# Optimization experiments

Hardware: AMD Instinct MI355X
Metric: run time of the kernel (lower is better)

Reference implementation:

```python
import jax, jax.numpy as jnp
import numpy as np
import math

EPS = 1e-5

def _ln(x, w, b):
    m = jnp.mean(x, axis=-1, keepdims=True)
    v = jnp.mean((x - m) ** 2, axis=-1, keepdims=True)
    return (x - m) * jax.lax.rsqrt(v + EPS) * w + b

def setup_inputs() -> dict:
    key = jax.random.key(0)
    L, E, V, T, B = 8, 1024, 32000, 1024, 4
    ks = jax.random.split(key, 9)
    f = lambda k, s: jax.random.normal(k, s, dtype=jnp.float32) * 0.02
    return dict(
        idx=jax.random.randint(ks[0], (B, T), 0, V),
        wte=f(ks[1], (V, E)),
        wpe=f(ks[2], (T, E)),
        ln1_w=jnp.ones((L, E), jnp.float32), ln1_b=jnp.zeros((L, E), jnp.float32),
        attn_w=f(ks[3], (L, 3 * E, E)), attn_b=jnp.zeros((L, 3 * E), jnp.float32),
        proj_w=f(ks[4], (L, E, E)), proj_b=jnp.zeros((L, E), jnp.float32),
        ln2_w=jnp.ones((L, E), jnp.float32), ln2_b=jnp.zeros((L, E), jnp.float32),
        fc_w=f(ks[5], (L, 4 * E, E)), fc_b=jnp.zeros((L, 4 * E), jnp.float32),
        fc2_w=f(ks[6], (L, E, 4 * E)), fc2_b=jnp.zeros((L, E), jnp.float32),
        lnf_w=jnp.ones((E,), jnp.float32), lnf_b=jnp.zeros((E,), jnp.float32),
        lm_head_w=f(ks[7], (V, E)),
        n_head=16,
    )

def reference(idx, wte, wpe, ln1_w, ln1_b, attn_w, attn_b, proj_w, proj_b,
              ln2_w, ln2_b, fc_w, fc_b, fc2_w, fc2_b, lnf_w, lnf_b,
              lm_head_w, n_head):
    B, T = idx.shape
    E = wte.shape[1]
    H = int(n_head)
    hd = E // H
    scale = 1.0 / math.sqrt(hd)
    x = wte[idx] + wpe[:T]  # [B,T,E]
    causal = jnp.tril(jnp.ones((T, T), dtype=bool))
    neg_inf = jnp.float32(-jnp.inf)

    def body(x, p):
        l1w, l1b, Wa, ba, Wp, bp, l2w, l2b, Wf, bf, W2, b2 = p
        h = _ln(x, l1w, l1b)
        qkv = h @ Wa.T + ba  # [B,T,3E]
        q, k, v = jnp.split(qkv, 3, axis=-1)
        q = q.reshape(B, T, H, hd)
        k = k.reshape(B, T, H, hd)
        v = v.reshape(B, T, H, hd)
        att = jnp.einsum('bqhd,bkhd->bhqk', q, k) * scale
        att = jnp.where(causal, att, neg_inf)
        att = jax.nn.softmax(att, axis=-1)  # dropout is identity in eval
        y = jnp.einsum('bhqk,bkhd->bqhd', att, v).reshape(B, T, E)
        x = x + (y @ Wp.T + bp)
        h2 = _ln(x, l2w, l2b)
        mlp = jax.nn.gelu(h2 @ Wf.T + bf, approximate=False) @ W2.T + b2
        return x + mlp, None

    params = (ln1_w, ln1_b, attn_w, attn_b, proj_w, proj_b,
              ln2_w, ln2_b, fc_w, fc_b, fc2_w, fc2_b)
    x, _ = jax.lax.scan(body, x, params)
    x = _ln(x, lnf_w, lnf_b)
    logits = x @ lm_head_w.T  # [B,T,V]
    return logits
```

## Files before the change

kernel.cpp:

```cpp
#include <hip/hip_runtime.h>

typedef __bf16 bf16x8 __attribute__((ext_vector_type(8)));
typedef float  f32x4  __attribute__((ext_vector_type(4)));
typedef short  s16x8  __attribute__((ext_vector_type(8)));
typedef unsigned int u32;
#define AS1 __attribute__((address_space(1)))
#define AS3 __attribute__((address_space(3)))

#define E_ 1024
#define T_ 1024
#define B_ 4
#define L_ 8
#define V_ 32000
#define M_ (B_*T_)

static __device__ __forceinline__ ushort f2bf(float f) {
  return __builtin_bit_cast(ushort, (__bf16)f);
}

static __device__ __forceinline__ bf16x8 dsr(const ushort* p) {
  u32 a = (u32)(size_t)(const AS3 ushort*)p;
  bf16x8 d;
  asm volatile("ds_read_b128 %0, %1" : "=v"(d) : "v"(a));
  return d;
}

__global__ __launch_bounds__(256) void castall_k(
    const float* __restrict__ a0, const float* __restrict__ a1,
    const float* __restrict__ a2, const float* __restrict__ a3,
    const float* __restrict__ a4,
    ushort* __restrict__ o0, ushort* __restrict__ o1, ushort* __restrict__ o2,
    ushort* __restrict__ o3, ushort* __restrict__ o4) {
  int bid = blockIdx.x;
  const float* in; ushort* out; int base;
  if (bid < 12288)      { in = a0; out = o0; base = bid; }
  else if (bid < 16384) { in = a1; out = o1; base = bid - 12288; }
  else if (bid < 32768) { in = a2; out = o2; base = bid - 16384; }
  else if (bid < 49152) { in = a3; out = o3; base = bid - 32768; }
  else                  { in = a4; out = o4; base = bid - 49152; }
  size_t i = ((size_t)base * 256 + threadIdx.x) * 8;
  float4 a = *(const float4*)(in + i);
  float4 b = *(const float4*)(in + i + 4);
  float v[8] = {a.x, a.y, a.z, a.w, b.x, b.y, b.z, b.w};
  union { s16x8 v; ushort u[8]; } pk;
  #pragma unroll
  for (int j = 0; j < 8; ++j) pk.u[j] = f2bf(v[j]);
  *(s16x8*)(out + i) = pk.v;
}

static __device__ __forceinline__ void ln_core(float4 v, int t,
    const float* __restrict__ w, const float* __restrict__ b,
    ushort* __restrict__ out, size_t row) {
  float s  = v.x + v.y + v.z + v.w;
  float s2 = v.x*v.x + v.y*v.y + v.z*v.z + v.w*v.w;
  #pragma unroll
  for (int o = 32; o > 0; o >>= 1) { s += __shfl_down(s, o); s2 += __shfl_down(s2, o); }
  __shared__ float sh[8];
  int wv = t >> 6;
  if ((t & 63) == 0) { sh[wv] = s; sh[4 + wv] = s2; }
  __syncthreads();
  s  = sh[0] + sh[1] + sh[2] + sh[3];
  s2 = sh[4] + sh[5] + sh[6] + sh[7];
  float mean = s * (1.f / E_);
  float var  = s2 * (1.f / E_) - mean * mean;
  float inv  = rsqrtf(var + 1e-5f);
  float4 wv4 = ((const float4*)w)[t];
  float4 bv4 = ((const float4*)b)[t];
  ushort* op = out + row * E_ + t * 4;
  op[0] = f2bf((v.x - mean) * inv * wv4.x + bv4.x);
  op[1] = f2bf((v.y - mean) * inv * wv4.y + bv4.y);
  op[2] = f2bf((v.z - mean) * inv * wv4.z + bv4.z);
  op[3] = f2bf((v.w - mean) * inv * wv4.w + bv4.w);
}

__global__ __launch_bounds__(256) void embedln_k(const int* __restrict__ idx,
    const float* __restrict__ wte, const float* __restrict__ wpe,
    const float* __restrict__ w, const float* __restrict__ b,
    float* __restrict__ x, ushort* __restrict__ out) {
  int row = blockIdx.x;
  int tok = idx[row];
  int t = row & (T_ - 1);
  int c = threadIdx.x;
  float4 a = ((const float4*)(wte + (size_t)tok * E_))[c];
  float4 p = ((const float4*)(wpe + (size_t)t * E_))[c];
  float4 v; v.x = a.x + p.x; v.y = a.y + p.y; v.z = a.z + p.z; v.w = a.w + p.w;
  ((float4*)(x + (size_t)row * E_))[c] = v;
  ln_core(v, c, w, b, out, (size_t)row);
}

__global__ __launch_bounds__(256) void ln_k(const float* __restrict__ x,
    const float* __restrict__ w, const float* __restrict__ b,
    ushort* __restrict__ out) {
  int row = blockIdx.x;
  int t = threadIdx.x;
  float4 v = ((const float4*)(x + (size_t)row * E_))[t];
  ln_core(v, t, w, b, out, (size_t)row);
}

__global__ __launch_bounds__(256) void redln_k(const float* __restrict__ p,
    const float* __restrict__ bias, float* __restrict__ x,
    const float* __restrict__ w, const float* __restrict__ b,
    ushort* __restrict__ out) {
  int row = blockIdx.x;
  int t = threadIdx.x;
  float4 v = ((const float4*)(x + (size_t)row * E_))[t];
  float4 bb = ((const float4*)bias)[t];
  v.x += bb.x; v.y += bb.y; v.z += bb.z; v.w += bb.w;
  #pragma unroll
  for (int sk = 0; sk < 4; ++sk) {
    float4 q = ((const float4*)(p + ((size_t)sk * M_ + row) * E_))[t];
    v.x += q.x; v.y += q.y; v.z += q.z; v.w += q.w;
  }
  ((float4*)(x + (size_t)row * E_))[t] = v;
  ln_core(v, t, w, b, out, (size_t)row);
}

template<int BUF, int MH, int NH, int RA, int RB, int VM, typename F>
static __device__ __forceinline__ void ph8(
    const ushort* AL, const ushort* BL,
    bf16x8 (&av)[2][4][2], bf16x8 (&bv)[2][2][2],
    int arow, int brow, int ca0, int ca1, f32x4 (&acc)[8][4], F&& stage) {
  if (RA) {
    #pragma unroll
    for (int mfi = 0; mfi < 4; ++mfi) {
      av[MH][mfi][0] = dsr(&AL[(BUF*2+MH)*8192 + arow + mfi*1024 + ca0]);
      av[MH][mfi][1] = dsr(&AL[(BUF*2+MH)*8192 + arow + mfi*1024 + ca1]);
    }
  }
  if (RB) {
    #pragma unroll
    for (int nfi = 0; nfi < 2; ++nfi) {
      bv[NH][nfi][0] = dsr(&BL[(BUF*2+NH)*8192 + brow + nfi*1024 + ca0]);
      bv[NH][nfi][1] = dsr(&BL[(BUF*2+NH)*8192 + brow + nfi*1024 + ca1]);
    }
  }
  stage();
  __builtin_amdgcn_s_barrier();
  asm volatile("s_waitcnt lgkmcnt(0)");
  __builtin_amdgcn_sched_barrier(0);
  __builtin_amdgcn_s_setprio(1);
  #pragma unroll
  for (int ks = 0; ks < 2; ++ks)
    #pragma unroll
    for (int mfi = 0; mfi < 4; ++mfi)
      #pragma unroll
      for (int nfi = 0; nfi < 2; ++nfi)
        acc[MH*4+mfi][NH*2+nfi] = __builtin_amdgcn_mfma_f32_16x16x32_bf16(
            av[MH][mfi][ks], bv[NH][nfi][ks], acc[MH*4+mfi][NH*2+nfi], 0, 0, 0);
  __builtin_amdgcn_s_setprio(0);
  if (VM) asm volatile("s_waitcnt vmcnt(4)");
  __builtin_amdgcn_s_barrier();
  __builtin_amdgcn_sched_barrier(0);
}

#define GLDS(src, dst) __builtin_amdgcn_global_load_lds((const AS1 u32*)(src), (AS3 u32*)(dst), 16, 0, 0)
#define STAGE_A(b, s, t) do { \
  GLDS(ap##s##_0 + (size_t)(t)*64, &AL[((b)*2+(s))*8192 + w*512]); \
  GLDS(ap##s##_1 + (size_t)(t)*64, &AL[((b)*2+(s))*8192 + 4096 + w*512]); } while(0)
#define STAGE_B(b, s, t) do { \
  GLDS(bp##s##_0 + (size_t)(t)*64, &BL[((b)*2+(s))*8192 + w*512]); \
  GLDS(bp##s##_1 + (size_t)(t)*64, &BL[((b)*2+(s))*8192 + 4096 + w*512]); } while(0)

template<int EPI>
static __device__ __forceinline__
void gemm8_body(const ushort* __restrict__ A, const ushort* __restrict__ W,
                const float* __restrict__ bias,
                float* __restrict__ outf, ushort* __restrict__ outh,
                ushort* __restrict__ qb, ushort* __restrict__ kb, ushort* __restrict__ vb,
                int M, int N, int K, int Kst) {
  __shared__ __align__(16) ushort AL[32768];
  __shared__ __align__(16) ushort BL[32768];
  int id  = blockIdx.x;
  int sk = 0, bx, by;
  if (EPI == 4) {
    sk = id >> 6; int rem = id & 63; bx = rem & 3; by = rem >> 2;
  } else {
    int nwg = gridDim.x;
    int swz = (id & 7) * (nwg >> 3) + (id >> 3);
    bx = swz >> 4; by = swz & 15;
  }
  int bm = by * 256, bn = bx * 256;
  int tid = threadIdx.x;
  int w = tid >> 6, lane = tid & 63;
  int wm = w >> 2, wn = w & 3;
  int g = lane >> 4, lr = lane & 15;
  int sl8 = lane >> 3, sc = lane & 7;
  int cg8 = (sc ^ sl8) * 8;

  const ushort* Ab = A + (size_t)sk * K;
  const ushort* Wb = W + (size_t)sk * K;
  int r0 = w * 8 + sl8;
  const ushort* ap0_0 = Ab + (size_t)(bm +       0 + r0) * Kst + cg8;
  const ushort* ap0_1 = Ab + (size_t)(bm + 128 + 0 + r0) * Kst + cg8;
  const ushort* ap1_0 = Ab + (size_t)(bm +      64 + r0) * Kst + cg8;
  const ushort* ap1_1 = Ab + (size_t)(bm + 128 + 64 + r0) * Kst + cg8;
  int sr0 = r0, sr1 = 64 + r0;
  const ushort* bp0_0 = Wb + (size_t)(bn + (sr0 >> 5) * 64 +  0 + (sr0 & 31)) * Kst + cg8;
  const ushort* bp0_1 = Wb + (size_t)(bn + (sr1 >> 5) * 64 +  0 + (sr1 & 31)) * Kst + cg8;
  const ushort* bp1_0 = Wb + (size_t)(bn + (sr0 >> 5) * 64 + 32 + (sr0 & 31)) * Kst + cg8;
  const ushort* bp1_1 = Wb + (size_t)(bn + (sr1 >> 5) * 64 + 32 + (sr1 & 31)) * Kst + cg8;

  int NT = K >> 6;
  int NITER = NT >> 1;
  int arow = (wm * 64 + lr) * 64;
  int brow = (wn * 32 + lr) * 64;
  int ca0 = ((0 + g) ^ (lr & 7)) * 8;
  int ca1 = ((4 + g) ^ (lr & 7)) * 8;
  f32x4 acc[8][4] = {};
  bf16x8 av[2][4][2], bv[2][2][2];

  STAGE_A(0, 0, 0); STAGE_A(0, 1, 0); STAGE_B(0, 0, 0); STAGE_B(0, 1, 0);
  STAGE_A(1, 0, 1); STAGE_B(1, 0, 1);
  asm volatile("s_waitcnt vmcnt(0)" ::: "memory");
  __builtin_amdgcn_s_barrier();
  __builtin_amdgcn_sched_barrier(0);

  for (int i = 0; i < NITER; ++i) {
    int t1 = 2 * i + 1;
    int t2 = 2 * i + 2; if (t2 > NT - 1) t2 = NT - 1;
    int t3 = 2 * i + 3; if (t3 > NT - 1) t3 = NT - 1;
    ph8<0,0,0,1,1,0>(AL, BL, av, bv, arow, brow, ca0, ca1, acc, [&]{ STAGE_A(1, 1, t1); });
    ph8<0,0,1,0,1,0>(AL, BL, av, bv, arow, brow, ca0, ca1, acc, [&]{ STAGE_B(1, 1, t1); });
    ph8<0,1,1,1,0,0>(AL, BL, av, bv, arow, brow, ca0, ca1, acc, [&]{ STAGE_A(0, 0, t2); });
    ph8<0,1,0,0,0,1>(AL, BL, av, bv, arow, brow, ca0, ca1, acc, [&]{ STAGE_B(0, 0, t2); });
    ph8<1,0,0,1,1,0>(AL, BL, av, bv, arow, brow, ca0, ca1, acc, [&]{ STAGE_A(0, 1, t2); });
    ph8<1,0,1,0,1,0>(AL, BL, av, bv, arow, brow, ca0, ca1, acc, [&]{ STAGE_B(0, 1, t2); });
    ph8<1,1,1,1,0,0>(AL, BL, av, bv, arow, brow, ca0, ca1, acc, [&]{ STAGE_A(1, 0, t3); });
    ph8<1,1,0,0,0,1>(AL, BL, av, bv, arow, brow, ca0, ca1, acc, [&]{ STAGE_B(1, 0, t3); });
  }

  if (EPI == 3 && (bn >> 10) == 2) {
    #pragma unroll
    for (int mf = 0; mf < 8; ++mf) {
      int row = bm + wm * 128 + mf * 16 + g * 4;
      int b = row >> 10, t = row & 1023;
      #pragma unroll
      for (int nf = 0; nf < 4; ++nf) {
        int col = bn + wn * 64 + nf * 16 + lr;
        int cc = col & 1023;
        int h = cc >> 6, d = cc & 63;
        float bs = bias[col];
        union { ushort u[4]; uint2 v; } pk4;
        #pragma unroll
        for (int reg = 0; reg < 4; ++reg) pk4.u[reg] = f2bf(acc[mf][nf][reg] + bs);
        *(uint2*)&vb[((size_t)(b * 16 + h) * 64 + d) * T_ + t] = pk4.v;
      }
    }
    return;
  }

  ushort* dst = nullptr; float scl = 1.f;
  if (EPI == 3) {
    int sec = bn >> 10;
    dst = (sec == 0) ? qb : kb;
    scl = (sec == 0) ? 0.125f : 1.f;
  }
  #pragma unroll
  for (int mf = 0; mf < 8; ++mf) {
    #pragma unroll
    for (int reg = 0; reg < 4; ++reg) {
      int row = bm + wm * 128 + mf * 16 + g * 4 + reg;
      #pragma unroll
      for (int nf = 0; nf < 4; ++nf) {
        int col = bn + wn * 64 + nf * 16 + lr;
        float v = acc[mf][nf][reg];
        if (bias) v += bias[col];
        if (EPI == 0) {
          outf[(size_t)row * N + col] = v;
        } else if (EPI == 2) {
          float gl = 0.5f * v * (1.f + erff(v * 0.70710678118654752f));
          outh[(size_t)row * N + col] = f2bf(gl);
        } else if (EPI == 4) {
          outf[((size_t)sk * M + row) * N + col] = v;
        } else {
          int b = row >> 10, t = row & 1023;
          int cc = col & 1023;
          int h = cc >> 6, d = cc & 63;
          dst[((size_t)(b * 16 + h) * T_ + t) * 64 + d] = f2bf(v * scl);
        }
      }
    }
  }
}

__global__ __launch_bounds__(512, 2)
void gemm8_qkv(const ushort* A, const ushort* W, const float* bias,
               ushort* qb, ushort* kb, ushort* vtb) {
  gemm8_body<3>(A, W, bias, nullptr, nullptr, qb, kb, vtb, M_, 3 * E_, E_, E_);
}
__global__ __launch_bounds__(512, 2)
void gemm8_fc(const ushort* A, const ushort* W, const float* bias, ushort* outh) {
  gemm8_body<2>(A, W, bias, nullptr, outh, nullptr, nullptr, nullptr, M_, 4 * E_, E_, E_);
}
__global__ __launch_bounds__(512, 2)
void gemm8_lm(const ushort* A, const ushort* W, float* outf) {
  gemm8_body<0>(A, W, nullptr, outf, nullptr, nullptr, nullptr, nullptr, M_, V_, E_, E_);
}
__global__ __launch_bounds__(512, 2)
void gemm8_sk(const ushort* A, const ushort* W, float* pbuf) {
  gemm8_body<4>(A, W, nullptr, pbuf, nullptr, nullptr, nullptr, nullptr, M_, E_, E_, 4 * E_);
}

__global__ __launch_bounds__(256, 4)
void gbt2_proj(const ushort* __restrict__ A, const ushort* __restrict__ W,
               const float* __restrict__ bias, const float* __restrict__ res,
               float* __restrict__ outf) {
  __shared__ __align__(16) ushort As[128 * 64];
  __shared__ __align__(16) ushort Ws[128 * 64];
  const int N = E_, K = E_;
  int id  = blockIdx.x;
  int nwg = gridDim.x;
  int swz = (id & 7) * (nwg >> 3) + (id >> 3);
  int bx = swz >> 5, by = swz & 31;
  int bm = by * 128, bn = bx * 128;
  int tid  = threadIdx.x;
  int wave = tid >> 6, lane = tid & 63;
  int wr = wave >> 1, wc = wave & 1;
  int g  = lane >> 4, lr = lane & 15;
  int sl8 = lane >> 3, sc = lane & 7;
  int cg8 = (sc ^ sl8) * 8;
  int r0 = wave * 8 + sl8;

  const ushort* ap = A + (size_t)(bm + r0) * K + cg8;
  const ushort* wp = W + (size_t)(bn + r0) * K + cg8;
  f32x4 acc[4][4] = {};

  for (int k0 = 0; k0 < K; k0 += 64) {
    #pragma unroll
    for (int j = 0; j < 4; ++j) {
      GLDS(ap + (size_t)(j * 32) * K + k0, &As[(wave * 8 + j * 32) * 64]);
      GLDS(wp + (size_t)(j * 32) * K + k0, &Ws[(wave * 8 + j * 32) * 64]);
    }
    __syncthreads();
    #pragma unroll
    for (int ks = 0; ks < 2; ++ks) {
      int ca = ((ks * 4 + g) ^ (lr & 7)) * 8;
      bf16x8 af[4], bfr[4];
      #pragma unroll
      for (int f = 0; f < 4; ++f) {
        af[f]  = __builtin_bit_cast(bf16x8, *(const s16x8*)&As[(wr * 64 + f * 16 + lr) * 64 + ca]);
        bfr[f] = __builtin_bit_cast(bf16x8, *(const s16x8*)&Ws[(wc * 64 + f * 16 + lr) * 64 + ca]);
      }
      #pragma unroll
      for (int mf = 0; mf < 4; ++mf)
        #pragma unroll
        for (int nf = 0; nf < 4; ++nf)
          acc[mf][nf] = __builtin_amdgcn_mfma_f32_16x16x32_bf16(af[mf], bfr[nf], acc[mf][nf], 0, 0, 0);
    }
    __syncthreads();
  }

  #pragma unroll
  for (int mf = 0; mf < 4; ++mf)
    #pragma unroll
    for (int reg = 0; reg < 4; ++reg) {
      int row = bm + wr * 64 + mf * 16 + g * 4 + reg;
      #pragma unroll
      for (int nf = 0; nf < 4; ++nf) {
        int col = bn + wc * 64 + nf * 16 + lr;
        float v = acc[mf][nf][reg] + bias[col];
        outf[(size_t)row * N + col] = v + res[(size_t)row * N + col];
      }
    }
}

static __device__ __forceinline__ void sm_step(
    f32x4 (&s)[4], float& m, float& l, f32x4 (&acc)[4], bf16x8 (&ap)[2],
    int qrow, int kbase0, bool diag, int g) {
  if (diag) {
    #pragma unroll
    for (int nf = 0; nf < 4; ++nf)
      #pragma unroll
      for (int reg = 0; reg < 4; ++reg)
        if (kbase0 + nf * 16 + g * 4 + reg > qrow) s[nf][reg] = -INFINITY;
  }
  float pmax = s[0][0];
  #pragma unroll
  for (int nf = 0; nf < 4; ++nf)
    #pragma unroll
    for (int reg = 0; reg < 4; ++reg) pmax = fmaxf(pmax, s[nf][reg]);
  pmax = fmaxf(pmax, __shfl_xor(pmax, 16));
  pmax = fmaxf(pmax, __shfl_xor(pmax, 32));
  if (__any(pmax > m + 8.f)) {
    float mn = fmaxf(m, pmax);
    float corr = __expf(m - mn);
    m = mn; l *= corr;
    #pragma unroll
    for (int reg = 0; reg < 4; ++reg) {
      float cc = __shfl(corr, g * 4 + reg);
      #pragma unroll
      for (int nfd = 0; nfd < 4; ++nfd) acc[nfd][reg] *= cc;
    }
  }
  float ps = 0.f;
  union { bf16x8 v[2]; ushort u[16]; } pk;
  #pragma unroll
  for (int nf = 0; nf < 4; ++nf)
    #pragma unroll
    for (int reg = 0; reg < 4; ++reg) {
      float pv = __expf(s[nf][reg] - m);
      ps += pv;
      pk.u[nf * 4 + reg] = f2bf(pv);
    }
  ps += __shfl_xor(ps, 16);
  ps += __shfl_xor(ps, 32);
  l += ps;
  ap[0] = pk.v[0];
  ap[1] = pk.v[1];
}

#define LOADK(dst, kt) do { \
  _Pragma("unroll") \
  for (int ks_ = 0; ks_ < 2; ++ks_) \
    _Pragma("unroll") \
    for (int nf_ = 0; nf_ < 4; ++nf_) \
      dst[ks_][nf_] = __builtin_bit_cast(bf16x8, *(const s16x8*)( \
          kbase + (size_t)((kt) * 64 + nf_ * 16 + lr) * 64 + ks_ * 32 + g * 8)); \
} while (0)

#define LOADV(dst, kt) do { \
  _Pragma("unroll") \
  for (int ks_ = 0; ks_ < 2; ++ks_) \
    _Pragma("unroll") \
    for (int nf_ = 0; nf_ < 4; ++nf_) { \
      const ushort* vp_ = vbase + (size_t)(nf_ * 16 + lr) * T_ + (kt) * 64 + ks_ * 32 + g * 4; \
      uint2 vlo_ = *(const uint2*)vp_; \
      uint2 vhi_ = *(const uint2*)(vp_ + 16); \
      union { uint4 u; bf16x8 v; } bb_; \
      bb_.u = make_uint4(vlo_.x, vlo_.y, vhi_.x, vhi_.y); \
      dst[ks_][nf_] = bb_.v; \
    } \
} while (0)

#define TILE(KF) do { \
  bool diag_ = (kt == nkt - 1); \
  f32x4 s0[4] = {}, s1[4] = {}; \
  _Pragma("unroll") \
  for (int ks_ = 0; ks_ < 2; ++ks_) \
    _Pragma("unroll") \
    for (int nf_ = 0; nf_ < 4; ++nf_) { \
      s0[nf_] = __builtin_amdgcn_mfma_f32_16x16x32_bf16(KF[ks_][nf_], aq[0][ks_], s0[nf_], 0, 0, 0); \
      s1[nf_] = __builtin_amdgcn_mfma_f32_16x16x32_bf16(KF[ks_][nf_], aq[1][ks_], s1[nf_], 0, 0, 0); \
    } \
  bf16x8 ap0[2], ap1[2]; \
  sm_step(s0, m0, l0, accO[0], ap0, qbase + 0 * 16 + lr, kt * 64, diag_, g); \
  sm_step(s1, m1, l1, accO[1], ap1, qbase + 1 * 16 + lr, kt * 64, diag_, g); \
  _Pragma("unroll") \
  for (int ks_ = 0; ks_ < 2; ++ks_) \
    _Pragma("unroll") \
    for (int nf_ = 0; nf_ < 4; ++nf_) { \
      accO[0][nf_] = __builtin_amdgcn_mfma_f32_16x16x32_bf16(ap0[ks_], vf[ks_][nf_], accO[0][nf_], 0, 0, 0); \
      accO[1][nf_] = __builtin_amdgcn_mfma_f32_16x16x32_bf16(ap1[ks_], vf[ks_][nf_], accO[1][nf_], 0, 0, 0); \
    } \
} while (0)

__global__ __launch_bounds__(64) void attn_k(const ushort* __restrict__ Qg,
    const ushort* __restrict__ Kg, const ushort* __restrict__ Vg,
    ushort* __restrict__ y) {
  int bh = blockIdx.x;
  int qt = blockIdx.y;
  int lane = threadIdx.x;
  int g = lane >> 4, lr = lane & 15;
  int qbase = qt * 32;

  const ushort* kbase = Kg + (size_t)bh * T_ * 64;
  const ushort* vbase = Vg + (size_t)bh * 64 * T_;

  bf16x8 aq[2][2];
  #pragma unroll
  for (int st = 0; st < 2; ++st) {
    const ushort* qp = Qg + ((size_t)bh * T_ + qbase + st * 16 + lr) * 64;
    aq[st][0] = __builtin_bit_cast(bf16x8, *(const s16x8*)(qp + g * 8));
    aq[st][1] = __builtin_bit_cast(bf16x8, *(const s16x8*)(qp + 32 + g * 8));
  }

  f32x4 accO[2][4] = {};
  float m0 = -INFINITY, m1 = -INFINITY, l0 = 0.f, l1 = 0.f;

  int nkt = (qbase >> 6) + 1;
  bf16x8 kA[2][4], kB[2][4], vf[2][4];
  LOADK(kA, 0);
  int kt = 0;
  for (;;) {
    LOADV(vf, kt);
    if (kt + 1 < nkt) LOADK(kB, kt + 1);
    TILE(kA);
    if (++kt >= nkt) break;
    LOADV(vf, kt);
    if (kt + 1 < nkt) LOADK(kA, kt + 1);
    TILE(kB);
    if (++kt >= nkt) break;
  }

  int b = bh >> 4, h = bh & 15;
  float li0 = 1.f / l0, li1 = 1.f / l1;
  #pragma unroll
  for (int st = 0; st < 2; ++st) {
    float lsrc = (st == 0) ? li0 : li1;
    #pragma unroll
    for (int reg = 0; reg < 4; ++reg) {
      float inv = __shfl(lsrc, g * 4 + reg);
      size_t row = (size_t)b * T_ + qbase + st * 16 + g * 4 + reg;
      #pragma unroll
      for (int nfd = 0; nfd < 4; ++nfd)
        y[row * E_ + h * 64 + nfd * 16 + lr] = f2bf(accO[st][nfd][reg] * inv);
    }
  }
}

extern "C" void kernel_launch(void* const* d_in, const int* in_sizes, int n_in,
                              void* d_out, int out_size, void* d_ws, size_t ws_size,
                              hipStream_t stream) {
  const int*   idx   = (const int*)  d_in[0];
  const float* wte   = (const float*)d_in[1];
  const float* wpe   = (const float*)d_in[2];
  const float* ln1w  = (const float*)d_in[3];
  const float* ln1b  = (const float*)d_in[4];
  const float* attnw = (const float*)d_in[5];
  const float* attnb = (const float*)d_in[6];
  const float* projw = (const float*)d_in[7];
  const float* projb = (const float*)d_in[8];
  const float* ln2w  = (const float*)d_in[9];
  const float* ln2b  = (const float*)d_in[10];
  const float* fcw   = (const float*)d_in[11];
  const float* fcb   = (const float*)d_in[12];
  const float* fc2w  = (const float*)d_in[13];
  const float* fc2b  = (const float*)d_in[14];
  const float* lnfw  = (const float*)d_in[15];
  const float* lnfb  = (const float*)d_in[16];
  const float* lmw   = (const float*)d_in[17];
  float* out = (float*)d_out;

  char* p = (char*)d_ws;
  auto take = [&](size_t bytes) { char* r = p; p += (bytes + 255) & ~(size_t)255; return r; };
  ushort* wb_attn = (ushort*)take((size_t)L_ * 3 * E_ * E_ * 2);
  ushort* wb_proj = (ushort*)take((size_t)L_ * E_ * E_ * 2);
  ushort* wb_fc   = (ushort*)take((size_t)L_ * 4 * E_ * E_ * 2);
  ushort* wb_fc2  = (ushort*)take((size_t)L_ * E_ * 4 * E_ * 2);
  ushort* wb_lm   = (ushort*)take((size_t)V_ * E_ * 2);
  float*  x       = (float*) take((size_t)M_ * E_ * 4);
  ushort* hbuf    = (ushort*)take((size_t)M_ * E_ * 2);
  ushort* qb      = (ushort*)take((size_t)B_ * 16 * T_ * 64 * 2);
  ushort* kbuf    = (ushort*)take((size_t)B_ * 16 * T_ * 64 * 2);
  ushort* vtb     = (ushort*)take((size_t)B_ * 16 * T_ * 64 * 2);
  ushort* ybuf    = (ushort*)take((size_t)M_ * E_ * 2);
  ushort* mlp     = (ushort*)take((size_t)M_ * 4 * E_ * 2);
  float*  pbuf    = (float*) take((size_t)4 * M_ * E_ * 4);

  castall_k<<<65152, 256, 0, stream>>>(attnw, projw, fcw, fc2w, lmw,
                                       wb_attn, wb_proj, wb_fc, wb_fc2, wb_lm);
  embedln_k<<<M_, 256, 0, stream>>>(idx, wte, wpe, ln1w, ln1b, x, hbuf);

  for (int l = 0; l < L_; ++l) {
    gemm8_qkv<<<(3 * E_ / 256) * (M_ / 256), 512, 0, stream>>>(
        hbuf, wb_attn + (size_t)l * 3 * E_ * E_, attnb + l * 3 * E_, qb, kbuf, vtb);
    attn_k<<<dim3(B_ * 16, 32), 64, 0, stream>>>(qb, kbuf, vtb, ybuf);
    gbt2_proj<<<(E_ / 128) * (M_ / 128), 256, 0, stream>>>(
        ybuf, wb_proj + (size_t)l * E_ * E_, projb + l * E_, x, x);
    ln_k<<<M_, 256, 0, stream>>>(x, ln2w + l * E_, ln2b + l * E_, hbuf);
    gemm8_fc<<<(4 * E_ / 256) * (M_ / 256), 512, 0, stream>>>(
        hbuf, wb_fc + (size_t)l * 4 * E_ * E_, fcb + l * 4 * E_, mlp);
    gemm8_sk<<<256, 512, 0, stream>>>(mlp, wb_fc2 + (size_t)l * E_ * 4 * E_, pbuf);
    if (l < L_ - 1)
      redln_k<<<M_, 256, 0, stream>>>(pbuf, fc2b + l * E_, x,
                                      ln1w + (l + 1) * E_, ln1b + (l + 1) * E_, hbuf);
    else
      redln_k<<<M_, 256, 0, stream>>>(pbuf, fc2b + l * E_, x, lnfw, lnfb, hbuf);
  }
  gemm8_lm<<<(V_ / 256) * (M_ / 256), 512, 0, stream>>>(hbuf, wb_lm, out);
}
```

Baseline: 2.516 ms.

## Share K/V tiles across four waves via double-buffered LDS in attention

The attention kernel moves from one 64-thread wave per 32 query rows to a 256-thread block covering 128 query rows. K and V tiles are staged into XOR-swizzled, double-buffered shared memory through global-to-LDS loads, so four waves reuse each tile instead of each fetching it from global memory. In exchange it adds block-wide barriers every key tile. Waves whose causal range is shorter sit idle while the block stages tiles for the longest wave, and the grid has four times fewer blocks.

```diff
diff --git a/kernel.cpp b/kernel.cpp
--- a/kernel.cpp
+++ b/kernel.cpp
@@ -409,59 +409,18 @@
   ap[1] = pk.v[1];
 }
 
-#define LOADK(dst, kt) do { \
-  _Pragma("unroll") \
-  for (int ks_ = 0; ks_ < 2; ++ks_) \
-    _Pragma("unroll") \
-    for (int nf_ = 0; nf_ < 4; ++nf_) \
-      dst[ks_][nf_] = __builtin_bit_cast(bf16x8, *(const s16x8*)( \
-          kbase + (size_t)((kt) * 64 + nf_ * 16 + lr) * 64 + ks_ * 32 + g * 8)); \
-} while (0)
-
-#define LOADV(dst, kt) do { \
-  _Pragma("unroll") \
-  for (int ks_ = 0; ks_ < 2; ++ks_) \
-    _Pragma("unroll") \
-    for (int nf_ = 0; nf_ < 4; ++nf_) { \
-      const ushort* vp_ = vbase + (size_t)(nf_ * 16 + lr) * T_ + (kt) * 64 + ks_ * 32 + g * 4; \
-      uint2 vlo_ = *(const uint2*)vp_; \
-      uint2 vhi_ = *(const uint2*)(vp_ + 16); \
-      union { uint4 u; bf16x8 v; } bb_; \
-      bb_.u = make_uint4(vlo_.x, vlo_.y, vhi_.x, vhi_.y); \
-      dst[ks_][nf_] = bb_.v; \
-    } \
-} while (0)
-
-#define TILE(KF) do { \
-  bool diag_ = (kt == nkt - 1); \
-  f32x4 s0[4] = {}, s1[4] = {}; \
-  _Pragma("unroll") \
-  for (int ks_ = 0; ks_ < 2; ++ks_) \
-    _Pragma("unroll") \
-    for (int nf_ = 0; nf_ < 4; ++nf_) { \
-      s0[nf_] = __builtin_amdgcn_mfma_f32_16x16x32_bf16(KF[ks_][nf_], aq[0][ks_], s0[nf_], 0, 0, 0); \
-      s1[nf_] = __builtin_amdgcn_mfma_f32_16x16x32_bf16(KF[ks_][nf_], aq[1][ks_], s1[nf_], 0, 0, 0); \
-    } \
-  bf16x8 ap0[2], ap1[2]; \
-  sm_step(s0, m0, l0, accO[0], ap0, qbase + 0 * 16 + lr, kt * 64, diag_, g); \
-  sm_step(s1, m1, l1, accO[1], ap1, qbase + 1 * 16 + lr, kt * 64, diag_, g); \
-  _Pragma("unroll") \
-  for (int ks_ = 0; ks_ < 2; ++ks_) \
-    _Pragma("unroll") \
-    for (int nf_ = 0; nf_ < 4; ++nf_) { \
-      accO[0][nf_] = __builtin_amdgcn_mfma_f32_16x16x32_bf16(ap0[ks_], vf[ks_][nf_], accO[0][nf_], 0, 0, 0); \
-      accO[1][nf_] = __builtin_amdgcn_mfma_f32_16x16x32_bf16(ap1[ks_], vf[ks_][nf_], accO[1][nf_], 0, 0, 0); \
-    } \
-} while (0)
-
-__global__ __launch_bounds__(64) void attn_k(const ushort* __restrict__ Qg,
+__global__ __launch_bounds__(256) void attn4_k(const ushort* __restrict__ Qg,
     const ushort* __restrict__ Kg, const ushort* __restrict__ Vg,
     ushort* __restrict__ y) {
+  __shared__ __align__(16) ushort KL[2][4096];
+  __shared__ __align__(16) ushort VL[2][4096];
   int bh = blockIdx.x;
   int qt = blockIdx.y;
-  int lane = threadIdx.x;
+  int tid = threadIdx.x, w = tid >> 6, lane = tid & 63;
   int g = lane >> 4, lr = lane & 15;
-  int qbase = qt * 32;
+  int sl8 = lane >> 3, sc = lane & 7;
+  int cg8 = (sc ^ sl8) * 8;
+  int qbase = qt * 128 + w * 32;
 
   const ushort* kbase = Kg + (size_t)bh * T_ * 64;
   const ushort* vbase = Vg + (size_t)bh * 64 * T_;
@@ -477,19 +436,58 @@
   f32x4 accO[2][4] = {};
   float m0 = -INFINITY, m1 = -INFINITY, l0 = 0.f, l1 = 0.f;
 
-  int nkt = (qbase >> 6) + 1;
-  bf16x8 kA[2][4], kB[2][4], vf[2][4];
-  LOADK(kA, 0);
-  int kt = 0;
-  for (;;) {
-    LOADV(vf, kt);
-    if (kt + 1 < nkt) LOADK(kB, kt + 1);
-    TILE(kA);
-    if (++kt >= nkt) break;
-    LOADV(vf, kt);
-    if (kt + 1 < nkt) LOADK(kA, kt + 1);
-    TILE(kB);
-    if (++kt >= nkt) break;
+  int nkt_blk = 2 * qt + 2;
+  int nw = ((qbase + 31) >> 6) + 1;
+  int r8 = w * 8 + sl8;
+
+  #define STG_KV(buf, kt) do { \
+    _Pragma("unroll") \
+    for (int j_ = 0; j_ < 2; ++j_) { \
+      GLDS(kbase + (size_t)((kt) * 64 + j_ * 32 + r8) * 64 + cg8, &KL[buf][(j_ * 32 + w * 8) * 64]); \
+      GLDS(vbase + (size_t)(j_ * 32 + r8) * T_ + (kt) * 64 + cg8, &VL[buf][(j_ * 32 + w * 8) * 64]); \
+    } \
+  } while (0)
+
+  STG_KV(0, 0);
+  __syncthreads();
+
+  for (int kt = 0; kt < nkt_blk; ++kt) {
+    int cbuf = kt & 1;
+    if (kt + 1 < nkt_blk) STG_KV(cbuf ^ 1, kt + 1);
+
+    if (kt < nw) {
+      bool diag = (kt == nw - 1);
+      f32x4 s0[4] = {}, s1[4] = {};
+      #pragma unroll
+      for (int ks = 0; ks < 2; ++ks)
+        #pragma unroll
+        for (int nf = 0; nf < 4; ++nf) {
+          int row = nf * 16 + lr;
+          bf16x8 ak = __builtin_bit_cast(bf16x8,
+              *(const s16x8*)&KL[cbuf][row * 64 + (((ks * 4 + g) ^ (lr & 7)) * 8)]);
+          s0[nf] = __builtin_amdgcn_mfma_f32_16x16x32_bf16(ak, aq[0][ks], s0[nf], 0, 0, 0);
+          s1[nf] = __builtin_amdgcn_mfma_f32_16x16x32_bf16(ak, aq[1][ks], s1[nf], 0, 0, 0);
+        }
+
+      bf16x8 ap0[2], ap1[2];
+      sm_step(s0, m0, l0, accO[0], ap0, qbase + 0 * 16 + lr, kt * 64, diag, g);
+      sm_step(s1, m1, l1, accO[1], ap1, qbase + 1 * 16 + lr, kt * 64, diag, g);
+
+      #pragma unroll
+      for (int ks = 0; ks < 2; ++ks)
+        #pragma unroll
+        for (int nfd = 0; nfd < 4; ++nfd) {
+          int row = nfd * 16 + lr;
+          int c1 = ks * 4 + (g >> 1), sub = (g & 1) * 4;
+          uint2 lo = *(const uint2*)&VL[cbuf][row * 64 + ((c1 ^ (lr & 7)) * 8 + sub)];
+          uint2 hi = *(const uint2*)&VL[cbuf][row * 64 + (((c1 + 2) ^ (lr & 7)) * 8 + sub)];
+          union { uint4 u; bf16x8 v; } bb;
+          bb.u = make_uint4(lo.x, lo.y, hi.x, hi.y);
+          accO[0][nfd] = __builtin_amdgcn_mfma_f32_16x16x32_bf16(ap0[ks], bb.v, accO[0][nfd], 0, 0, 0);
+          accO[1][nfd] = __builtin_amdgcn_mfma_f32_16x16x32_bf16(ap1[ks], bb.v, accO[1][nfd], 0, 0, 0);
+        }
+    }
+    __syncthreads();
   }
 
   int b = bh >> 4, h = bh & 15;
@@ -506,6 +504,7 @@
         y[row * E_ + h * 64 + nfd * 16 + lr] = f2bf(accO[st][nfd][reg] * inv);
     }
   }
+  #undef STG_KV
 }
 
 extern "C" void kernel_launch(void* const* d_in, const int* in_sizes, int n_in,
@@ -554,7 +553,7 @@
   for (int l = 0; l < L_; ++l) {
     gemm8_qkv<<<(3 * E_ / 256) * (M_ / 256), 512, 0, stream>>>(
         hbuf, wb_attn + (size_t)l * 3 * E_ * E_, attnb + l * 3 * E_, qb, kbuf, vtb);
-    attn_k<<<dim3(B_ * 16, 32), 64, 0, stream>>>(qb, kbuf, vtb, ybuf);
+    attn4_k<<<dim3(B_ * 16, T_ / 128), 256, 0, stream>>>(qb, kbuf, vtb, ybuf);
     gbt2_proj<<<(E_ / 128) * (M_ / 128), 256, 0, stream>>>(
         ybuf, wb_proj + (size_t)l * E_ * E_, projb + l * E_, x, x);
     ln_k<<<M_, 256, 0, stream>>>(x, ln2w + l * E_, ln2b + l * E_, hbuf);
```

After: 2.350 ms. -6.6%, faster.
